# Optimization experiments

Hardware: AMD Instinct MI355X
Metric: run time of the kernel (lower is better)

The kernel has to match this reference:

```python
import jax, jax.numpy as jnp
import numpy as np

EPS = 1e-5
K = 3  # fixed kernel_size in the module


def _conv(x, w, pad):
    return jax.lax.conv_general_dilated(
        x, w, (1, 1), [(pad, pad), (pad, pad)],
        dimension_numbers=('NCHW', 'OIHW', 'NCHW'))


def _bn(x, g, b, m, v):
    # inference-mode BatchNorm2d with running stats
    scale = g / jnp.sqrt(v + EPS)
    return x * scale[None, :, None, None] + (b - m * scale)[None, :, None, None]


def _unfold3(x):
    # x: [B,C,H,W] -> [B,C,9,H,W]; kernel positions row-major, matching nn.Unfold
    H, W = x.shape[2], x.shape[3]
    xp = jnp.pad(x, ((0, 0), (0, 0), (1, 1), (1, 1)))
    return jnp.stack([xp[:, :, i:i + H, j:j + W]
                      for i in range(K) for j in range(K)], axis=2)


def setup_inputs() -> dict:
    key = jax.random.key(0)
    ks = jax.random.split(key, 9)
    B, C, H, W = 8, 64, 128, 128
    Cr = C // 4           # reduce channels = 16
    KN = K * K * 2        # kernel_num = 18 (groups = 2)
    guide_feat = jax.random.normal(ks[0], (B, C, H, W), jnp.float32)
    target_feat = jax.random.normal(ks[1], (B, C, H, W), jnp.float32)
    w_reduce = jax.random.normal(ks[2], (Cr, C, 1, 1), jnp.float32) * 0.1
    bn1_g = jnp.ones((Cr,), jnp.float32)
    bn1_b = jnp.zeros((Cr,), jnp.float32)
    bn1_m = jax.random.normal(ks[3], (Cr,), jnp.float32) * 0.1
    bn1_v = jax.random.uniform(ks[4], (Cr,), jnp.float32, 0.5, 1.5)
    w_span = jax.random.normal(ks[5], (KN, Cr, 1, 1), jnp.float32) * 0.1
    b_span = jnp.zeros((KN,), jnp.float32)
    w_bconv = jax.random.normal(ks[6], (C, C, 3, 3), jnp.float32) * 0.05
    bn3_g = jnp.ones((C,), jnp.float32)
    bn3_b = jnp.zeros((C,), jnp.float32)
    bn3_m = jax.random.normal(ks[7], (C,), jnp.float32) * 0.1
    bn3_v = jax.random.uniform(ks[8], (C,), jnp.float32, 0.5, 1.5)
    return dict(guide_feat=guide_feat, target_feat=target_feat,
                w_reduce=w_reduce, bn1_g=bn1_g, bn1_b=bn1_b, bn1_m=bn1_m, bn1_v=bn1_v,
                w_span=w_span, b_span=b_span,
                w_bconv=w_bconv, bn3_g=bn3_g, bn3_b=bn3_b, bn3_m=bn3_m, bn3_v=bn3_v)


def reference(guide_feat, target_feat, w_reduce, bn1_g, bn1_b, bn1_m, bn1_v,
              w_span, b_span, w_bconv, bn3_g, bn3_b, bn3_m, bn3_v):
    B, C, H, W = target_feat.shape
    groups = 2
    gc = C // 2  # group_channels
    # kernel generation branch
    x = guide_feat + target_feat
    x = jax.nn.relu(_bn(_conv(x, w_reduce, 0), bn1_g, bn1_b, bn1_m, bn1_v))
    kern = _conv(x, w_span, 0) + b_span[None, :, None, None]  # [B,18,H,W]
    kern = kern.reshape(B, groups, K * K, H, W)
    # involution: unfold target, multiply by per-pixel kernels, sum over window
    patches = _unfold3(target_feat).reshape(B, groups, gc, K * K, H, W)
    out = jnp.einsum('bgkhw,bgckhw->bgchw', kern, patches).reshape(B, C, H, W)
    # final 3x3 ConvBNReLU
    return jax.nn.relu(_bn(_conv(out, w_bconv, 1), bn3_g, bn3_b, bn3_m, bn3_v))
```

## Files before the change

### kernel.cpp

```cpp
#include <hip/hip_runtime.h>

#define B_  8
#define C_  64
#define H_  128
#define W_  128
#define HW_ (H_*W_)
#define NP_ ((size_t)B_*HW_)

typedef __attribute__((ext_vector_type(4)))  float f32x4;
typedef __attribute__((ext_vector_type(16))) float f32x16;
typedef __attribute__((ext_vector_type(8)))  short short8;

static __device__ __forceinline__ unsigned short f2bf(float f) {
  unsigned int u = __float_as_uint(f);
  u += 0x7fff + ((u >> 16) & 1);
  return (unsigned short)(u >> 16);
}
static __device__ __forceinline__ float bf2f(unsigned short u) {
  return __uint_as_float((unsigned int)u << 16);
}

__global__ void k0_prep(const float* __restrict__ w, const float* __restrict__ wred,
                        const float* __restrict__ g3, const float* __restrict__ b3,
                        const float* __restrict__ m3, const float* __restrict__ v3,
                        unsigned short* __restrict__ afrag,
                        unsigned short* __restrict__ afrag_red,
                        float* __restrict__ s3, float* __restrict__ sh3) {
  int idx = blockIdx.x * 256 + threadIdx.x;
  if (idx < 36864) {
    int j    = idx & 7;
    int lane = (idx >> 3) & 63;
    int fs   = idx >> 9;
    int ks16 = fs & 3;
    int kk   = (fs >> 2) % 9;
    int mh   = fs / 36;
    int oc = mh * 32 + (lane & 31);
    int ic = ks16 * 16 + (lane >> 5) * 8 + j;
    afrag[idx] = f2bf(w[(oc * 64 + ic) * 9 + kk]);
  } else if (idx < 38912) {
    int i2 = idx - 36864;
    int j    = i2 & 7;
    int lane = (i2 >> 3) & 63;
    int ks   = i2 >> 9;
    int m  = lane & 31;
    int ic = ks * 16 + (lane >> 5) * 8 + j;
    afrag_red[i2] = (m < 16) ? f2bf(wred[m * 64 + ic]) : (unsigned short)0;
  } else if (idx < 38976) {
    int c = idx - 38912;
    float s = g3[c] * rsqrtf(v3[c] + 1e-5f);
    s3[c]  = s;
    sh3[c] = b3[c] - m3[c] * s;
  }
}

__global__ __launch_bounds__(512, 4) void k1_fused(
    const float* __restrict__ guide, const float* __restrict__ target,
    const unsigned short* __restrict__ afrag_red,
    const float* __restrict__ bn1g, const float* __restrict__ bn1b,
    const float* __restrict__ bn1m, const float* __restrict__ bn1v,
    const float* __restrict__ w_span, const float* __restrict__ b_span,
    unsigned short* __restrict__ inv) {
  __shared__ __align__(16) unsigned short t16[324 * 64];
  __shared__ f32x4 s_wspan[18][4];
  __shared__ f32x4 s_s1v[4], s_sh1v[4];
  __shared__ float s_bsp[18];
  int t = threadIdx.x;
  if (t < 288) {
    int j = t >> 4, r = t & 15;
    ((float*)&s_wspan[j][0])[r] = w_span[t];
  }
  if (t < 16) {
    float s = bn1g[t] * rsqrtf(bn1v[t] + 1e-5f);
    ((float*)s_s1v)[t]  = s;
    ((float*)s_sh1v)[t] = bn1b[t] - bn1m[t] * s;
  }
  if (t < 18) s_bsp[t] = b_span[t];

  int b  = blockIdx.z;
  int h0 = blockIdx.y * 16, w0 = blockIdx.x * 16;
  const float* tb = target + (size_t)b * C_ * HW_;

  for (int i = t; i < 2592; i += 512) {
    int c8 = i / 324, cell = i - c8 * 324;
    int r = cell / 18, col = cell - r * 18;
    int hh = h0 + r - 1, ww = w0 + col - 1;
    short8 val = {0, 0, 0, 0, 0, 0, 0, 0};
    if ((unsigned)hh < (unsigned)H_ && (unsigned)ww < (unsigned)W_) {
      const float* src = tb + (size_t)(c8 * 8) * HW_ + hh * W_ + ww;
      #pragma unroll
      for (int ci = 0; ci < 8; ++ci) val[ci] = (short)f2bf(src[(size_t)ci * HW_]);
    }
    *(short8*)&t16[cell * 64 + ((c8 ^ (cell & 7)) * 8)] = val;
  }

  int wave = t >> 6, l = t & 63, h = l >> 5;
  short8 a_red[4];
  #pragma unroll
  for (int ks = 0; ks < 4; ++ks)
    a_red[ks] = *(const short8*)(afrag_red + ((size_t)(ks * 64 + l)) * 8);
  __syncthreads();

  int p   = wave * 32 + (l & 31);
  int tyP = p >> 4, txP = p & 15;
  const float* gpx = guide + (size_t)b * C_ * HW_ + (h0 + tyP) * W_ + (w0 + txP);
  int cellC = (tyP + 1) * 18 + (txP + 1);

  f32x16 xa;
  #pragma unroll
  for (int i = 0; i < 16; ++i) xa[i] = 0.f;
  #pragma unroll
  for (int ks = 0; ks < 4; ++ks) {
    short8 tvv = *(const short8*)&t16[cellC * 64 + (((2 * ks + h) ^ (cellC & 7)) * 8)];
    int ch0 = ks * 16 + h * 8;
    short8 bf;
    #pragma unroll
    for (int j = 0; j < 8; ++j)
      bf[j] = (short)f2bf(gpx[(size_t)(ch0 + j) * HW_] + bf2f((unsigned short)tvv[j]));
    xa = __builtin_amdgcn_mfma_f32_32x32x16_bf16(a_red[ks], bf, xa, 0, 0, 0);
  }
  f32x4 x0, x1;
  #pragma unroll
  for (int r = 0; r < 4; ++r) { x0[r] = xa[r]; x1[r] = xa[4 + r]; }
  {
    f32x4 sA = s_s1v[h], shA = s_sh1v[h], sB = s_s1v[2 + h], shB = s_sh1v[2 + h];
    #pragma unroll
    for (int r = 0; r < 4; ++r) {
      x0[r] = fmaxf(x0[r] * sA[r] + shA[r], 0.f);
      x1[r] = fmaxf(x1[r] * sB[r] + shB[r], 0.f);
    }
  }

  float kg[9];
  #pragma unroll
  for (int j9 = 0; j9 < 9; ++j9) {
    int jA = h * 9 + j9;
    int jB = (9 - 9 * h) + j9;
    f32x4 wA0 = s_wspan[jA][h],     wA1 = s_wspan[jA][2 + h];
    f32x4 wB0 = s_wspan[jB][h],     wB1 = s_wspan[jB][2 + h];
    float pa = 0.f, pb = 0.f;
    #pragma unroll
    for (int r = 0; r < 4; ++r) {
      pa += wA0[r] * x0[r] + wA1[r] * x1[r];
      pb += wB0[r] * x0[r] + wB1[r] * x1[r];
    }
    float recv = __shfl_xor(pb, 32, 64);
    kg[j9] = pa + recv + s_bsp[jA];
  }

  size_t pix = ((size_t)b * H_ + (h0 + tyP)) * W_ + (w0 + txP);
  #pragma unroll
  for (int i = 0; i < 4; ++i) {
    int c8 = h * 4 + i;
    float a8[8];
    #pragma unroll
    for (int ci = 0; ci < 8; ++ci) a8[ci] = 0.f;
    #pragma unroll
    for (int di = 0; di < 3; ++di) {
      #pragma unroll
      for (int dj = 0; dj < 3; ++dj) {
        int cell = (tyP + di) * 18 + (txP + dj);
        short8 tv = *(const short8*)&t16[cell * 64 + ((c8 ^ (cell & 7)) * 8)];
        float k = kg[di * 3 + dj];
        #pragma unroll
        for (int ci = 0; ci < 8; ++ci) a8[ci] += k * bf2f((unsigned short)tv[ci]);
      }
    }
    short8 pv;
    #pragma unroll
    for (int ci = 0; ci < 8; ++ci) pv[ci] = (short)f2bf(a8[ci]);
    *(short8*)(inv + ((size_t)c8 * NP_ + pix) * 8) = pv;
  }
}

__global__ __launch_bounds__(256, 4) void k2_conv(
    const unsigned short* __restrict__ inv, const unsigned short* __restrict__ afrag,
    const float* __restrict__ s3g, const float* __restrict__ sh3g,
    float* __restrict__ out) {
  __shared__ __align__(16) unsigned short tile[204 * 64];
  int t = threadIdx.x;
  int b  = blockIdx.z;
  int h0 = blockIdx.y * 4;
  int w0 = blockIdx.x * 32;

  #pragma unroll
  for (int chunk = 0; chunk < 8; ++chunk) {
    if (t < 204) {
      int r = t / 34, col = t - r * 34;
      int hh = h0 + r - 1, ww = w0 + col - 1;
      short8 val = {0, 0, 0, 0, 0, 0, 0, 0};
      if ((unsigned)hh < (unsigned)H_ && (unsigned)ww < (unsigned)W_)
        val = *(const short8*)(inv + ((size_t)chunk * NP_ + ((size_t)b * H_ + hh) * W_ + ww) * 8);
      *(short8*)&tile[t * 64 + ((chunk ^ (col & 7)) * 8)] = val;
    }
  }

  int wave = t >> 6, lane = t & 63;
  int mh = wave & 1;
  int rp = (wave >> 1) * 2;
  __syncthreads();

  f32x16 acc0, acc1;
  #pragma unroll
  for (int i = 0; i < 16; ++i) { acc0[i] = 0.f; acc1[i] = 0.f; }

  for (int kk = 0; kk < 9; ++kk) {
    int di = kk / 3, dj = kk - di * 3;
    const unsigned short* ap = afrag + (((size_t)(mh * 9 + kk) * 4) * 64 + lane) * 8;
    short8 A0 = *(const short8*)(ap);
    short8 A1 = *(const short8*)(ap + 512);
    short8 A2 = *(const short8*)(ap + 1024);
    short8 A3 = *(const short8*)(ap + 1536);
    int col = (lane & 31) + dj;
    int swb = (lane >> 5);
    int cb0 = (rp + di) * 34 + col;
    #pragma unroll
    for (int ks = 0; ks < 4; ++ks) {
      int sw = ((ks * 2 + swb) ^ (col & 7)) * 8;
      short8 b0 = *(const short8*)&tile[cb0 * 64 + sw];
      short8 b1 = *(const short8*)&tile[(cb0 + 34) * 64 + sw];
      short8 Ak = (ks == 0) ? A0 : (ks == 1) ? A1 : (ks == 2) ? A2 : A3;
      acc0 = __builtin_amdgcn_mfma_f32_32x32x16_bf16(Ak, b0, acc0, 0, 0, 0);
      acc1 = __builtin_amdgcn_mfma_f32_32x32x16_bf16(Ak, b1, acc1, 0, 0, 0);
    }
  }

  int wcol = lane & 31;
  #pragma unroll
  for (int reg = 0; reg < 16; ++reg) {
    int oc = mh * 32 + (reg & 3) + 8 * (reg >> 2) + 4 * (lane >> 5);
    float s  = s3g[oc];
    float sh = sh3g[oc];
    float* op = out + ((size_t)b * C_ + oc) * HW_ + (h0 + rp) * W_ + w0 + wcol;
    op[0]  = fmaxf(acc0[reg] * s + sh, 0.f);
    op[W_] = fmaxf(acc1[reg] * s + sh, 0.f);
  }
}

extern "C" void kernel_launch(void* const* d_in, const int* in_sizes, int n_in,
                              void* d_out, int out_size, void* d_ws, size_t ws_size,
                              hipStream_t stream) {
  const float* guide    = (const float*)d_in[0];
  const float* target   = (const float*)d_in[1];
  const float* w_reduce = (const float*)d_in[2];
  const float* bn1g     = (const float*)d_in[3];
  const float* bn1b     = (const float*)d_in[4];
  const float* bn1m     = (const float*)d_in[5];
  const float* bn1v     = (const float*)d_in[6];
  const float* w_span   = (const float*)d_in[7];
  const float* b_span   = (const float*)d_in[8];
  const float* w_bconv  = (const float*)d_in[9];
  const float* bn3g     = (const float*)d_in[10];
  const float* bn3b     = (const float*)d_in[11];
  const float* bn3m     = (const float*)d_in[12];
  const float* bn3v     = (const float*)d_in[13];
  float* out = (float*)d_out;

  unsigned short* afrag     = (unsigned short*)d_ws;
  unsigned short* afrag_red = (unsigned short*)((char*)d_ws + 81920);
  float* s3  = (float*)((char*)d_ws + 90112);
  float* sh3 = (float*)((char*)d_ws + 90368);
  unsigned short* inv = (unsigned short*)((char*)d_ws + (1 << 17));

  hipLaunchKernelGGL(k0_prep, dim3(153), dim3(256), 0, stream,
                     w_bconv, w_reduce, bn3g, bn3b, bn3m, bn3v,
                     afrag, afrag_red, s3, sh3);
  hipLaunchKernelGGL(k1_fused, dim3(W_ / 16, H_ / 16, B_), dim3(512), 0, stream,
                     guide, target, afrag_red, bn1g, bn1b, bn1m, bn1v,
                     w_span, b_span, inv);
  hipLaunchKernelGGL(k2_conv, dim3(W_ / 32, H_ / 4, B_), dim3(256), 0, stream,
                     inv, afrag, s3, sh3, out);
}
```

Baseline: 164.5 us.

## Retile involution kernel to 4x32 rows with vectorized row-wise halo loads

Changes k1 from 16x16 tiles with 512 threads to 4x32 tiles with 256 threads. The halo tile (6x36 cells) is loaded as float4 runs along rows per channel, replacing scattered scalar loads that gathered 8 channels per cell. The aim is coalesced, vectorized global reads of the target tensor. In exchange the halo overhead per pixel is larger, and the LDS writes become scalar 16-bit stores that may bank-conflict.

```diff
diff --git a/kernel.cpp b/kernel.cpp
--- a/kernel.cpp
+++ b/kernel.cpp
@@ -53,21 +53,21 @@
   }
 }
 
-__global__ __launch_bounds__(512, 4) void k1_fused(
+__global__ __launch_bounds__(256, 4) void k1_fused(
     const float* __restrict__ guide, const float* __restrict__ target,
     const unsigned short* __restrict__ afrag_red,
     const float* __restrict__ bn1g, const float* __restrict__ bn1b,
     const float* __restrict__ bn1m, const float* __restrict__ bn1v,
     const float* __restrict__ w_span, const float* __restrict__ b_span,
     unsigned short* __restrict__ inv) {
-  __shared__ __align__(16) unsigned short t16[324 * 64];
+  __shared__ __align__(16) unsigned short t16[216 * 64];
   __shared__ f32x4 s_wspan[18][4];
   __shared__ f32x4 s_s1v[4], s_sh1v[4];
   __shared__ float s_bsp[18];
   int t = threadIdx.x;
-  if (t < 288) {
-    int j = t >> 4, r = t & 15;
-    ((float*)&s_wspan[j][0])[r] = w_span[t];
+  for (int i = t; i < 288; i += 256) {
+    int j = i >> 4, r = i & 15;
+    ((float*)&s_wspan[j][0])[r] = w_span[i];
   }
   if (t < 16) {
     float s = bn1g[t] * rsqrtf(bn1v[t] + 1e-5f);
@@ -77,20 +77,29 @@
   if (t < 18) s_bsp[t] = b_span[t];
 
   int b  = blockIdx.z;
-  int h0 = blockIdx.y * 16, w0 = blockIdx.x * 16;
+  int r0 = blockIdx.y * 4;
+  int w0 = blockIdx.x * 32;
   const float* tb = target + (size_t)b * C_ * HW_;
 
-  for (int i = t; i < 2592; i += 512) {
-    int c8 = i / 324, cell = i - c8 * 324;
-    int r = cell / 18, col = cell - r * 18;
-    int hh = h0 + r - 1, ww = w0 + col - 1;
-    short8 val = {0, 0, 0, 0, 0, 0, 0, 0};
-    if ((unsigned)hh < (unsigned)H_ && (unsigned)ww < (unsigned)W_) {
-      const float* src = tb + (size_t)(c8 * 8) * HW_ + hh * W_ + ww;
+  for (int i = t; i < 384; i += 256) {
+    int tr = i >> 6, c = i & 63;
+    int gr = r0 - 1 + tr;
+    bool rv = (unsigned)gr < (unsigned)H_;
+    const float* src = tb + (size_t)c * HW_ + gr * W_;
+    #pragma unroll
+    for (int j = 0; j < 10; ++j) {
+      int g0 = w0 - 4 + 4 * j;
+      f32x4 v = {0.f, 0.f, 0.f, 0.f};
+      if (rv && g0 >= 0 && g0 <= W_ - 4) v = *(const f32x4*)(src + g0);
       #pragma unroll
-      for (int ci = 0; ci < 8; ++ci) val[ci] = (short)f2bf(src[(size_t)ci * HW_]);
-    }
-    *(short8*)&t16[cell * 64 + ((c8 ^ (cell & 7)) * 8)] = val;
+      for (int e = 0; e < 4; ++e) {
+        int lc = 4 * j + e - 2;
+        if (lc >= 0 && lc < 36) {
+          int cell = tr * 36 + lc;
+          t16[cell * 64 + (((c >> 3) ^ (cell & 7)) * 8) + (c & 7)] = f2bf(v[e]);
+        }
+      }
+    }
   }
 
   int wave = t >> 6, l = t & 63, h = l >> 5;
@@ -100,10 +109,9 @@
     a_red[ks] = *(const short8*)(afrag_red + ((size_t)(ks * 64 + l)) * 8);
   __syncthreads();
 
-  int p   = wave * 32 + (l & 31);
-  int tyP = p >> 4, txP = p & 15;
-  const float* gpx = guide + (size_t)b * C_ * HW_ + (h0 + tyP) * W_ + (w0 + txP);
-  int cellC = (tyP + 1) * 18 + (txP + 1);
+  int ty = wave, tx = l & 31;
+  const float* gpx = guide + (size_t)b * C_ * HW_ + (r0 + ty) * W_ + (w0 + tx);
+  int cellC = (ty + 1) * 36 + (tx + 2);
 
   f32x16 xa;
   #pragma unroll
@@ -135,8 +143,8 @@
   for (int j9 = 0; j9 < 9; ++j9) {
     int jA = h * 9 + j9;
     int jB = (9 - 9 * h) + j9;
-    f32x4 wA0 = s_wspan[jA][h],     wA1 = s_wspan[jA][2 + h];
-    f32x4 wB0 = s_wspan[jB][h],     wB1 = s_wspan[jB][2 + h];
+    f32x4 wA0 = s_wspan[jA][h], wA1 = s_wspan[jA][2 + h];
+    f32x4 wB0 = s_wspan[jB][h], wB1 = s_wspan[jB][2 + h];
     float pa = 0.f, pb = 0.f;
     #pragma unroll
     for (int r = 0; r < 4; ++r) {
@@ -147,7 +155,7 @@
     kg[j9] = pa + recv + s_bsp[jA];
   }
 
-  size_t pix = ((size_t)b * H_ + (h0 + tyP)) * W_ + (w0 + txP);
+  size_t pix = ((size_t)b * H_ + (r0 + ty)) * W_ + (w0 + tx);
   #pragma unroll
   for (int i = 0; i < 4; ++i) {
     int c8 = h * 4 + i;
@@ -158,7 +166,7 @@
     for (int di = 0; di < 3; ++di) {
       #pragma unroll
       for (int dj = 0; dj < 3; ++dj) {
-        int cell = (tyP + di) * 18 + (txP + dj);
+        int cell = (ty + di) * 36 + (tx + dj + 1);
         short8 tv = *(const short8*)&t16[cell * 64 + ((c8 ^ (cell & 7)) * 8)];
         float k = kg[di * 3 + dj];
         #pragma unroll
@@ -264,7 +272,7 @@
   hipLaunchKernelGGL(k0_prep, dim3(153), dim3(256), 0, stream,
                      w_bconv, w_reduce, bn3g, bn3b, bn3m, bn3v,
                      afrag, afrag_red, s3, sh3);
-  hipLaunchKernelGGL(k1_fused, dim3(W_ / 16, H_ / 16, B_), dim3(512), 0, stream,
+  hipLaunchKernelGGL(k1_fused, dim3(W_ / 32, H_ / 4, B_), dim3(256), 0, stream,
                      guide, target, afrag_red, bn1g, bn1b, bn1m, bn1v,
                      w_span, b_span, inv);
   hipLaunchKernelGGL(k2_conv, dim3(W_ / 32, H_ / 4, B_), dim3(256), 0, stream,
```

New measurement: 184.8 us. +12.3%, slower.

## Load conv B-operands directly from global memory instead of LDS tile

Applied to the files above, without the earlier changes.

The 3x3 conv kernel drops its shared-memory halo tile and the block barrier. Each wave now loads its bf16 B fragments straight from global memory (through cache) with clamped addresses and zero masking, and the kk loop is fully unrolled. This removes LDS staging, the barrier and the LDS footprint, which may raise occupancy, but adds redundant global/L2 traffic because each input is re-read for all nine taps and by both M-half waves.

```diff
diff --git a/kernel.cpp b/kernel.cpp
--- a/kernel.cpp
+++ b/kernel.cpp
@@ -135,8 +135,8 @@
   for (int j9 = 0; j9 < 9; ++j9) {
     int jA = h * 9 + j9;
     int jB = (9 - 9 * h) + j9;
-    f32x4 wA0 = s_wspan[jA][h],     wA1 = s_wspan[jA][2 + h];
-    f32x4 wB0 = s_wspan[jB][h],     wB1 = s_wspan[jB][2 + h];
+    f32x4 wA0 = s_wspan[jA][h], wA1 = s_wspan[jA][2 + h];
+    f32x4 wB0 = s_wspan[jB][h], wB1 = s_wspan[jB][2 + h];
     float pa = 0.f, pb = 0.f;
     #pragma unroll
     for (int r = 0; r < 4; ++r) {
@@ -176,51 +176,47 @@
     const unsigned short* __restrict__ inv, const unsigned short* __restrict__ afrag,
     const float* __restrict__ s3g, const float* __restrict__ sh3g,
     float* __restrict__ out) {
-  __shared__ __align__(16) unsigned short tile[204 * 64];
   int t = threadIdx.x;
+  int wave = t >> 6, lane = t & 63;
+  int mh = wave & 1;
+  int rp = (wave >> 1) * 2;
   int b  = blockIdx.z;
   int h0 = blockIdx.y * 4;
   int w0 = blockIdx.x * 32;
-
-  #pragma unroll
-  for (int chunk = 0; chunk < 8; ++chunk) {
-    if (t < 204) {
-      int r = t / 34, col = t - r * 34;
-      int hh = h0 + r - 1, ww = w0 + col - 1;
-      short8 val = {0, 0, 0, 0, 0, 0, 0, 0};
-      if ((unsigned)hh < (unsigned)H_ && (unsigned)ww < (unsigned)W_)
-        val = *(const short8*)(inv + ((size_t)chunk * NP_ + ((size_t)b * H_ + hh) * W_ + ww) * 8);
-      *(short8*)&tile[t * 64 + ((chunk ^ (col & 7)) * 8)] = val;
-    }
-  }
-
-  int wave = t >> 6, lane = t & 63;
-  int mh = wave & 1;
-  int rp = (wave >> 1) * 2;
-  __syncthreads();
+  int tx = lane & 31, hb = lane >> 5;
 
   f32x16 acc0, acc1;
   #pragma unroll
   for (int i = 0; i < 16; ++i) { acc0[i] = 0.f; acc1[i] = 0.f; }
 
+  const size_t bbase = (size_t)b * H_;
+  const short8 z = {0, 0, 0, 0, 0, 0, 0, 0};
+
+  #pragma unroll
   for (int kk = 0; kk < 9; ++kk) {
-    int di = kk / 3, dj = kk - di * 3;
+    const int di = kk / 3, dj = kk - di * 3;
     const unsigned short* ap = afrag + (((size_t)(mh * 9 + kk) * 4) * 64 + lane) * 8;
-    short8 A0 = *(const short8*)(ap);
-    short8 A1 = *(const short8*)(ap + 512);
-    short8 A2 = *(const short8*)(ap + 1024);
-    short8 A3 = *(const short8*)(ap + 1536);
-    int col = (lane & 31) + dj;
-    int swb = (lane >> 5);
-    int cb0 = (rp + di) * 34 + col;
+    int wj = w0 + tx + dj - 1;
+    bool cok = (unsigned)wj < (unsigned)W_;
+    int wc = min(max(wj, 0), W_ - 1);
+    int hr0 = h0 + rp + di - 1;
+    int hr1 = hr0 + 1;
+    bool r0ok = cok && ((unsigned)hr0 < (unsigned)H_);
+    bool r1ok = cok && ((unsigned)hr1 < (unsigned)H_);
+    int hc0 = min(max(hr0, 0), H_ - 1);
+    int hc1 = min(max(hr1, 0), H_ - 1);
+    size_t p0 = (bbase + hc0) * W_ + wc;
+    size_t p1 = (bbase + hc1) * W_ + wc;
     #pragma unroll
     for (int ks = 0; ks < 4; ++ks) {
-      int sw = ((ks * 2 + swb) ^ (col & 7)) * 8;
-      short8 b0 = *(const short8*)&tile[cb0 * 64 + sw];
-      short8 b1 = *(const short8*)&tile[(cb0 + 34) * 64 + sw];
-      short8 Ak = (ks == 0) ? A0 : (ks == 1) ? A1 : (ks == 2) ? A2 : A3;
-      acc0 = __builtin_amdgcn_mfma_f32_32x32x16_bf16(Ak, b0, acc0, 0, 0, 0);
-      acc1 = __builtin_amdgcn_mfma_f32_32x32x16_bf16(Ak, b1, acc1, 0, 0, 0);
+      int c8 = ks * 2 + hb;
+      short8 A  = *(const short8*)(ap + (size_t)ks * 512);
+      short8 v0 = *(const short8*)(inv + ((size_t)c8 * NP_ + p0) * 8);
+      short8 v1 = *(const short8*)(inv + ((size_t)c8 * NP_ + p1) * 8);
+      short8 b0 = r0ok ? v0 : z;
+      short8 b1 = r1ok ? v1 : z;
+      acc0 = __builtin_amdgcn_mfma_f32_32x32x16_bf16(A, b0, acc0, 0, 0, 0);
+      acc1 = __builtin_amdgcn_mfma_f32_32x32x16_bf16(A, b1, acc1, 0, 0, 0);
     }
   }
 
```

After: 167.4 us. About the same (+1.8%).
